# Kernel optimization log

Hardware: AMD Instinct MI355X
Metric: run time of the kernel (lower is better)

The kernel has to match this reference:

```python
import jax, jax.numpy as jnp
import numpy as np

B, N, C = 8, 1025, 1024
H = 8
D = C // H  # 128
LORA = 16
TOK = 1024

def setup_inputs() -> dict:
    key = jax.random.key(0)
    ks = jax.random.split(key, 16)
    s = 0.02
    return {
        "x": jax.random.normal(ks[0], (B, N, C), jnp.float32),
        "style_k": jax.random.normal(ks[1], (B, N, C), jnp.float32),
        "style_v": jax.random.normal(ks[2], (B, N, C), jnp.float32),
        "W_qkv": jax.random.normal(ks[3], (C, 3 * C), jnp.float32) * s,
        "W_proj": jax.random.normal(ks[4], (C, C), jnp.float32) * s,
        "b_proj": jnp.zeros((C,), jnp.float32),
        "ak": jax.random.normal(ks[5], (TOK, LORA), jnp.float32) * s,
        "bk": jax.random.normal(ks[6], (LORA, C), jnp.float32) * s,
        "av": jax.random.normal(ks[7], (TOK, LORA), jnp.float32) * s,
        "bv": jax.random.normal(ks[8], (LORA, C), jnp.float32) * s,
        "W1": jax.random.normal(ks[9], (C, C // 4), jnp.float32) * s,
        "b1": jnp.zeros((C // 4,), jnp.float32),
        "W2": jax.random.normal(ks[10], (C // 4, 1), jnp.float32) * s,
        "b2": jnp.zeros((1,), jnp.float32),
    }

def reference(x, style_k, style_v, W_qkv, W_proj, b_proj, ak, bk, av, bv, W1, b1, W2, b2):
    Bx, Nx, Cx = x.shape
    # cls-token gating MLP over transposed patch tokens: cp has shape [B, C, N-1], N-1 == C
    cls_token = x[:, :1, :]                         # [B,1,C]
    cp = jnp.transpose(x[:, 1:, :], (0, 2, 1))      # [B,C,N-1]
    h = jax.nn.relu(cp @ W1 + b1)                   # [B,C,C//4]
    attn_w = jax.nn.sigmoid(h @ W2 + b2)            # [B,C,1]
    attn_w = attn_w[..., 0][:, None, :]             # [B,1,C]
    weighted_cls = cls_token * attn_w               # [B,1,C]

    qkv = (x @ W_qkv).reshape(Bx, Nx, 3, H, D)
    q, k, v = qkv[:, :, 0], qkv[:, :, 1], qkv[:, :, 2]  # each [B,N,H,D]

    tokens_k = ak @ bk                              # [TOK, C] (TOK == C)
    tokens_v = av @ bv
    lora_k = (style_k @ tokens_k.T).reshape(Bx, Nx, H, D)
    lora_v = (style_v @ tokens_v.T).reshape(Bx, Nx, H, D)

    kk = k + lora_k
    vv = v + lora_v
    scale = D ** -0.5  # xformers default softmax scale
    scores = jnp.einsum('bqhd,bkhd->bhqk', q, kk) * scale
    attn = jax.nn.softmax(scores, axis=-1)
    out = jnp.einsum('bhqk,bkhd->bqhd', attn, vv).reshape(Bx, Nx, Cx)
    out = out @ W_proj + b_proj

    x_return = jnp.concatenate([out[:, :1, :] + weighted_cls, out[:, 1:, :]], axis=1)
    return (x_return, vv)
```

## Files before the change

### kernel.cpp

```cpp
#include <hip/hip_runtime.h>
#include <hip/hip_bf16.h>
#include <stdint.h>

#define B_ 8
#define N_ 1025
#define C_ 1024
#define H_ 8
#define D_ 128
#define TOK_ 1024
#define LORA_ 16
#define M_ 8200
#define NPAD_ 1032

using bf16x8 = __attribute__((ext_vector_type(8))) short;
using f32x4  = __attribute__((ext_vector_type(4))) float;
typedef unsigned short u16;

__device__ __forceinline__ u16 f2bf(float f) {
    union { float f; unsigned u; } v; v.f = f;
    unsigned r = v.u + 0x7fffu + ((v.u >> 16) & 1u);
    return (u16)(r >> 16);
}

__device__ __forceinline__ unsigned cvt_pk_bf16(float lo, float hi) {
    unsigned r;
    asm("v_cvt_pk_bf16_f32 %0, %1, %2" : "=v"(r) : "v"(lo), "v"(hi));
    return r;
}

__device__ __forceinline__ void gload16(const u16* g, u16* l) {
    __builtin_amdgcn_global_load_lds(
        (const __attribute__((address_space(1))) void*)g,
        (__attribute__((address_space(3))) void*)l, 16, 0, 0);
}

__device__ __forceinline__ int xcd_swz(int bid, int nwg) {
    int cpx = nwg >> 3;
    return (bid & 7) * cpx + (bid >> 3);
}

__global__ __launch_bounds__(256) void cast3_kernel(
    const float* __restrict__ x, const float* __restrict__ sk, const float* __restrict__ sv,
    u16* __restrict__ xb, u16* __restrict__ skb, u16* __restrict__ svb)
{
    const float* in = blockIdx.y == 0 ? x : (blockIdx.y == 1 ? sk : sv);
    u16* out = blockIdx.y == 0 ? xb : (blockIdx.y == 1 ? skb : svb);
    size_t i = (size_t)blockIdx.x * 256 + threadIdx.x;
    float4 a = *((const float4*)in + i * 2);
    float4 b = *((const float4*)in + i * 2 + 1);
    bf16x8 v;
    v[0] = (short)f2bf(a.x); v[1] = (short)f2bf(a.y);
    v[2] = (short)f2bf(a.z); v[3] = (short)f2bf(a.w);
    v[4] = (short)f2bf(b.x); v[5] = (short)f2bf(b.y);
    v[6] = (short)f2bf(b.z); v[7] = (short)f2bf(b.w);
    *(bf16x8*)(out + i * 8) = v;
}

__global__ __launch_bounds__(256) void padcast16_kernel(
    const float* __restrict__ ak, const float* __restrict__ av,
    u16* __restrict__ akp, u16* __restrict__ avp)
{
    const float* in = blockIdx.y ? av : ak;
    u16* out = blockIdx.y ? avp : akp;
    int i = blockIdx.x * 256 + threadIdx.x;
    int t = i >> 4, l = i & 15;
    out[(size_t)t * 32 + l] = f2bf(in[i]);
    out[(size_t)t * 32 + 16 + l] = 0;
}

__global__ __launch_bounds__(256) void castb_kernel(
    const float* __restrict__ bk, const float* __restrict__ bv,
    u16* __restrict__ bkb, u16* __restrict__ bvb)
{
    const float* in = blockIdx.y ? bv : bk;
    u16* out = blockIdx.y ? bvb : bkb;
    int i = blockIdx.x * 256 + threadIdx.x;
    out[i] = f2bf(in[i]);
}

__global__ __launch_bounds__(256) void lora16_mfma(
    const u16* __restrict__ skb, const u16* __restrict__ svb,
    const u16* __restrict__ bkb, const u16* __restrict__ bvb,
    u16* __restrict__ sk16p, u16* __restrict__ sv16p)
{
    const u16* sb = blockIdx.y ? svb : skb;
    const u16* bb = blockIdx.y ? bvb : bkb;
    u16* op = blockIdx.y ? sv16p : sk16p;
    const int lane = threadIdx.x & 63, wid = threadIdx.x >> 6;
    const int base = blockIdx.x * 64 + wid * 16;
    int ma = base + (lane & 15); if (ma > M_ - 1) ma = M_ - 1;
    const int l = lane & 15;
    const u16* arow = sb + (size_t)ma * C_ + (lane >> 4) * 8;
    const u16* brow = bb + (size_t)l * C_ + (lane >> 4) * 8;
    f32x4 acc = {0.f, 0.f, 0.f, 0.f};
#pragma unroll
    for (int k0 = 0; k0 < C_; k0 += 32) {
        bf16x8 af = *(const bf16x8*)(arow + k0);
        bf16x8 bf = *(const bf16x8*)(brow + k0);
        acc = __builtin_amdgcn_mfma_f32_16x16x32_bf16(af, bf, acc, 0, 0, 0);
    }
#pragma unroll
    for (int r = 0; r < 4; ++r) {
        int m = base + (lane >> 4) * 4 + r; if (m > M_ - 1) m = M_ - 1;
        op[(size_t)m * 32 + l] = f2bf(acc[r]);
        op[(size_t)m * 32 + 16 + l] = 0;
    }
}

__global__ __launch_bounds__(256) void wt_kernel(
    const float* __restrict__ in, u16* __restrict__ out, int K, int Nw)
{
    __shared__ float t[32][33];
    int n0 = blockIdx.x * 32, k0 = blockIdx.y * 32;
    int tx = threadIdx.x & 31, ty = threadIdx.x >> 5;
#pragma unroll
    for (int yy = 0; yy < 32; yy += 8)
        t[ty + yy][tx] = in[(size_t)(k0 + ty + yy) * Nw + n0 + tx];
    __syncthreads();
#pragma unroll
    for (int yy = 0; yy < 32; yy += 8)
        out[(size_t)(n0 + ty + yy) * K + k0 + tx] = f2bf(t[tx][ty + yy]);
}

__global__ __launch_bounds__(256) void xt_kernel(
    const float* __restrict__ x, u16* __restrict__ xT)
{
    __shared__ float tb[32][33];
    int t0 = blockIdx.x * 32, c0 = blockIdx.y * 32, b = blockIdx.z;
    int tx = threadIdx.x & 31, ty = threadIdx.x >> 5;
#pragma unroll
    for (int yy = 0; yy < 32; yy += 8)
        tb[ty + yy][tx] = x[((size_t)b * N_ + 1 + t0 + ty + yy) * C_ + c0 + tx];
    __syncthreads();
#pragma unroll
    for (int yy = 0; yy < 32; yy += 8)
        xT[((size_t)b * 1024 + c0 + ty + yy) * 1024 + t0 + tx] = f2bf(tb[tx][ty + yy]);
}

__global__ __launch_bounds__(256) void vvt_kernel(
    const float* __restrict__ vv, u16* __restrict__ vvT)
{
    __shared__ float t[32][33];
    int n0 = blockIdx.x * 32, d0 = blockIdx.y * 32, bh = blockIdx.z;
    int b = bh >> 3, h = bh & 7;
    int tx = threadIdx.x & 31, ty = threadIdx.x >> 5;
#pragma unroll
    for (int yy = 0; yy < 32; yy += 8) {
        int n = n0 + ty + yy; if (n > 1024) n = 1024;
        t[ty + yy][tx] = vv[((size_t)(b * N_) + n) * C_ + h * D_ + d0 + tx];
    }
    __syncthreads();
#pragma unroll
    for (int yy = 0; yy < 32; yy += 8) {
        int n = n0 + tx;
        if (n < NPAD_)
            vvT[((size_t)bh * D_ + d0 + ty + yy) * NPAD_ + n] = f2bf(t[tx][ty + yy]);
    }
}

__device__ __forceinline__ void stage_tile(
    const u16* __restrict__ base, int row0, int maxrow,
    u16* lds, int k0, int lane, int wid)
{
#pragma unroll
    for (int j = 0; j < 4; ++j) {
        int i = wid * 4 + j;
        int p = i * 1024 + 16 * lane;
        int row = p >> 7, cb = p & 127;
        int cbs = cb ^ ((row & 7) << 4);
        int gr = row0 + row; if (gr > maxrow) gr = maxrow;
        gload16(base + (size_t)gr * 1024 + k0 + (cbs >> 1), lds + i * 512);
    }
}

__device__ __forceinline__ void gemm_pass(
    const u16* __restrict__ A, const u16* __restrict__ Bt, int row0, int nb0,
    u16* As, u16* Bs, f32x4 acc[4][4],
    const int lane, const int wid, const int wr, const int wc)
{
    for (int k0 = 0; k0 < 1024; k0 += 64) {
        __syncthreads();
        stage_tile(A,  row0, M_ - 1,    As, k0, lane, wid);
        stage_tile(Bt, nb0,  (1 << 30), Bs, k0, lane, wid);
        __syncthreads();
#pragma unroll
        for (int ks = 0; ks < 2; ++ks) {
            bf16x8 af[4], bfr[4];
#pragma unroll
            for (int mi = 0; mi < 4; ++mi) {
                int r = wr * 64 + mi * 16 + (lane & 15);
                int byte = (r * 128 + ks * 64 + (lane >> 4) * 16) ^ ((r & 7) << 4);
                af[mi] = *(const bf16x8*)((const char*)As + byte);
            }
#pragma unroll
            for (int ni = 0; ni < 4; ++ni) {
                int r = wc * 64 + ni * 16 + (lane & 15);
                int byte = (r * 128 + ks * 64 + (lane >> 4) * 16) ^ ((r & 7) << 4);
                bfr[ni] = *(const bf16x8*)((const char*)Bs + byte);
            }
#pragma unroll
            for (int mi = 0; mi < 4; ++mi)
#pragma unroll
                for (int ni = 0; ni < 4; ++ni)
                    acc[mi][ni] = __builtin_amdgcn_mfma_f32_16x16x32_bf16(
                        af[mi], bfr[ni], acc[mi][ni], 0, 0, 0);
        }
    }
}

__global__ __launch_bounds__(256) void se_gemm(
    const u16* __restrict__ xT, const u16* __restrict__ W1T,
    const float* __restrict__ b1, const float* __restrict__ W2,
    const float* __restrict__ b2, const float* __restrict__ x,
    float* __restrict__ wcls)
{
    __shared__ u16 As[8192], Bs[8192];
    __shared__ float red[128];
    const int tid = threadIdx.x, lane = tid & 63, wid = tid >> 6;
    const int wr = wid >> 1, wc = wid & 1;
    const int row0 = blockIdx.x * 128;
    if (tid < 128) red[tid] = 0.f;
    const f32x4 FZ = {0.f, 0.f, 0.f, 0.f};

#pragma unroll
    for (int pass = 0; pass < 2; ++pass) {
        f32x4 acc[4][4];
#pragma unroll
        for (int mi = 0; mi < 4; ++mi)
#pragma unroll
            for (int ni = 0; ni < 4; ++ni) acc[mi][ni] = FZ;
        gemm_pass(xT, W1T, row0, pass * 128, As, Bs, acc, lane, wid, wr, wc);
#pragma unroll
        for (int mi = 0; mi < 4; ++mi) {
#pragma unroll
            for (int r = 0; r < 4; ++r) {
                float v = 0.f;
#pragma unroll
                for (int ni = 0; ni < 4; ++ni) {
                    int j = pass * 128 + wc * 64 + ni * 16 + (lane & 15);
                    float h = acc[mi][ni][r] + b1[j];
                    v += fmaxf(h, 0.f) * W2[j];
                }
#pragma unroll
                for (int off = 1; off < 16; off <<= 1) v += __shfl_xor(v, off);
                if ((lane & 15) == 0)
                    atomicAdd(&red[wr * 64 + mi * 16 + (lane >> 4) * 4 + r], v);
            }
        }
    }
    __syncthreads();
    if (tid < 128) {
        int row = row0 + tid;
        int b = row >> 10, c = row & 1023;
        float aw = 1.f / (1.f + expf(-(red[tid] + b2[0])));
        wcls[row] = x[(size_t)b * N_ * C_ + c] * aw;
    }
}

__global__ __launch_bounds__(256) void qkv_gemm(
    const u16* __restrict__ xb, const u16* __restrict__ WqkvT,
    const u16* __restrict__ sk16p, const u16* __restrict__ sv16p,
    const u16* __restrict__ akp, const u16* __restrict__ avp,
    u16* __restrict__ qb, u16* __restrict__ kkb, float* __restrict__ vvout)
{
    __shared__ u16 As[8192], Bs[8192];
    const int tid = threadIdx.x, lane = tid & 63, wid = tid >> 6;
    const int wr = wid >> 1, wc = wid & 1;
    const int swz = xcd_swz(blockIdx.x, 65 * 24);
    const int row0 = (swz / 24) * 128;
    const int ct = swz % 24, region = ct >> 3;
    const int creg = (ct & 7) * 128;
    const f32x4 FZ = {0.f, 0.f, 0.f, 0.f};
    f32x4 acc[4][4];
#pragma unroll
    for (int mi = 0; mi < 4; ++mi)
#pragma unroll
        for (int ni = 0; ni < 4; ++ni) acc[mi][ni] = FZ;

    gemm_pass(xb, WqkvT, row0, ct * 128, As, Bs, acc, lane, wid, wr, wc);

    if (region >= 1) {
        const u16* a16 = (region == 1) ? sk16p : sv16p;
        const u16* b16 = (region == 1) ? akp : avp;
        bf16x8 af2[4], bf2v[4];
#pragma unroll
        for (int mi = 0; mi < 4; ++mi) {
            int gr = row0 + wr * 64 + mi * 16 + (lane & 15);
            if (gr > M_ - 1) gr = M_ - 1;
            af2[mi] = *(const bf16x8*)(a16 + (size_t)gr * 32 + (lane >> 4) * 8);
        }
#pragma unroll
        for (int ni = 0; ni < 4; ++ni) {
            int gc = creg + wc * 64 + ni * 16 + (lane & 15);
            bf2v[ni] = *(const bf16x8*)(b16 + (size_t)gc * 32 + (lane >> 4) * 8);
        }
#pragma unroll
        for (int mi = 0; mi < 4; ++mi)
#pragma unroll
            for (int ni = 0; ni < 4; ++ni)
                acc[mi][ni] = __builtin_amdgcn_mfma_f32_16x16x32_bf16(
                    af2[mi], bf2v[ni], acc[mi][ni], 0, 0, 0);
    }

#pragma unroll
    for (int mi = 0; mi < 4; ++mi) {
#pragma unroll
        for (int r = 0; r < 4; ++r) {
            int gr = row0 + wr * 64 + mi * 16 + (lane >> 4) * 4 + r;
            if (gr >= M_) continue;
#pragma unroll
            for (int ni = 0; ni < 4; ++ni) {
                int gc = creg + wc * 64 + ni * 16 + (lane & 15);
                float v = acc[mi][ni][r];
                if (region == 0)      qb [(size_t)gr * C_ + gc] = f2bf(v);
                else if (region == 1) kkb[(size_t)gr * C_ + gc] = f2bf(v);
                else                  vvout[(size_t)gr * C_ + gc] = v;
            }
        }
    }
}

__global__ __launch_bounds__(256) void proj_gemm(
    const u16* __restrict__ ob, const u16* __restrict__ WprojT,
    const float* __restrict__ bias, const float* __restrict__ wcls,
    float* __restrict__ outp)
{
    __shared__ u16 As[8192], Bs[8192];
    const int tid = threadIdx.x, lane = tid & 63, wid = tid >> 6;
    const int wr = wid >> 1, wc = wid & 1;
    const int swz = xcd_swz(blockIdx.x, 65 * 8);
    const int row0 = (swz / 8) * 128;
    const int ct = swz % 8;
    const f32x4 FZ = {0.f, 0.f, 0.f, 0.f};
    f32x4 acc[4][4];
#pragma unroll
    for (int mi = 0; mi < 4; ++mi)
#pragma unroll
        for (int ni = 0; ni < 4; ++ni) acc[mi][ni] = FZ;

    gemm_pass(ob, WprojT, row0, ct * 128, As, Bs, acc, lane, wid, wr, wc);

#pragma unroll
    for (int mi = 0; mi < 4; ++mi) {
#pragma unroll
        for (int r = 0; r < 4; ++r) {
            int gr = row0 + wr * 64 + mi * 16 + (lane >> 4) * 4 + r;
            if (gr >= M_) continue;
#pragma unroll
            for (int ni = 0; ni < 4; ++ni) {
                int gc = ct * 128 + wc * 64 + ni * 16 + (lane & 15);
                float v = acc[mi][ni][r] + bias[gc];
                if (gr % N_ == 0) v += wcls[(gr / N_) * C_ + gc];
                outp[(size_t)gr * C_ + gc] = v;
            }
        }
    }
}

__device__ __forceinline__ void stageK(
    const u16* __restrict__ kbase, u16* Ksb, int kv0, int lane, int wid)
{
#pragma unroll
    for (int j = 0; j < 4; ++j) {
        int i = wid * 4 + j;
        int p = i * 1024 + 16 * lane;
        int row = p >> 8, cb = p & 255;
        int cbs = cb ^ ((row & 7) << 4);
        int n = kv0 + row; if (n > 1024) n = 1024;
        gload16(kbase + (size_t)n * C_ + (cbs >> 1), Ksb + i * 512);
    }
}
__device__ __forceinline__ void stageV(
    const u16* __restrict__ vbase, u16* Vsb, int kv0, int lane, int wid)
{
#pragma unroll
    for (int j = 0; j < 4; ++j) {
        int i = wid * 4 + j;
        int p = i * 1024 + 16 * lane;
        int row = p >> 7, cb = p & 127;
        int cbs = cb ^ ((row & 7) << 4);
        int st = kv0 + (cbs >> 1); if (st > NPAD_ - 8) st = NPAD_ - 8;
        gload16(vbase + (size_t)row * NPAD_ + st, Vsb + i * 512);
    }
}

__global__ __launch_bounds__(256) void attn_kernel(
    const u16* __restrict__ qb, const u16* __restrict__ kkb,
    const u16* __restrict__ vvT, u16* __restrict__ ob)
{
    __shared__ u16 Ks[2][8192];
    __shared__ u16 Vs[8192];
    __shared__ u16 Ps[4096];
    const int tid = threadIdx.x, lane = tid & 63, wid = tid >> 6;
    const int swz = xcd_swz(blockIdx.x, 17 * 64);
    const int qt = swz % 17, bh = swz / 17, b = bh >> 3, h = bh & 7;
    const int n0q = qt * 64;
    const float C2 = 0.1275006182f;
    const u16* kbase = kkb + (size_t)b * N_ * C_ + h * D_;
    const u16* vbase = vvT + (size_t)bh * D_ * NPAD_;

    bf16x8 qf[4];
    {
        int qrow = n0q + wid * 16 + (lane & 15); if (qrow > 1024) qrow = 1024;
        const u16* qbase = qb + (size_t)(b * N_ + qrow) * C_ + h * D_ + (lane >> 4) * 8;
#pragma unroll
        for (int ks = 0; ks < 4; ++ks) qf[ks] = *(const bf16x8*)(qbase + ks * 32);
    }

    const bf16x8 ones = {0x3F80, 0x3F80, 0x3F80, 0x3F80, 0x3F80, 0x3F80, 0x3F80, 0x3F80};
    float mrow[4];
    const f32x4 FZ = {0.f, 0.f, 0.f, 0.f};
    f32x4 of[8], lsacc = FZ;
#pragma unroll
    for (int r = 0; r < 4; ++r) mrow[r] = -3e38f;
#pragma unroll
    for (int ct = 0; ct < 8; ++ct) of[ct] = FZ;

    char* psb = (char*)Ps + wid * 2048;

    stageK(kbase, Ks[0], 0, lane, wid);

    for (int t = 0; t < 17; ++t) {
        const int cur = t & 1;
        const int kv0 = t * 64;
        asm volatile("s_waitcnt vmcnt(0)" ::: "memory");
        __builtin_amdgcn_s_barrier();
        __builtin_amdgcn_sched_barrier(0);
        stageV(vbase, Vs, kv0, lane, wid);
        if (t < 16) stageK(kbase, Ks[cur ^ 1], kv0 + 64, lane, wid);

        f32x4 s[4];
        __builtin_amdgcn_s_setprio(1);
#pragma unroll
        for (int jt = 0; jt < 4; ++jt) {
            f32x4 a = FZ;
#pragma unroll
            for (int ks = 0; ks < 4; ++ks) {
                int kvr = jt * 16 + (lane & 15);
                int byte = (kvr * 256 + ks * 64 + (lane >> 4) * 16) ^ ((kvr & 7) << 4);
                bf16x8 kf = *(const bf16x8*)((const char*)Ks[cur] + byte);
                a = __builtin_amdgcn_mfma_f32_16x16x32_bf16(qf[ks], kf, a, 0, 0, 0);
            }
            s[jt] = a;
        }
        __builtin_amdgcn_s_setprio(0);
#pragma unroll
        for (int jt = 0; jt < 4; ++jt) {
            f32x4 a = s[jt] * C2;
            int kvglob = kv0 + jt * 16 + (lane & 15);
            if (kvglob > 1024) { a[0] = -3e38f; a[1] = -3e38f; a[2] = -3e38f; a[3] = -3e38f; }
            s[jt] = a;
        }

        float tm[4];
        int need = 0;
#pragma unroll
        for (int r = 0; r < 4; ++r) {
            float t0 = fmaxf(fmaxf(s[0][r], s[1][r]), fmaxf(s[2][r], s[3][r]));
#pragma unroll
            for (int off = 1; off < 16; off <<= 1) t0 = fmaxf(t0, __shfl_xor(t0, off));
            tm[r] = t0;
            need |= (t0 > mrow[r] + 11.54f) ? 1 : 0;
        }
        if (__any(need)) {
            float al[4];
#pragma unroll
            for (int r = 0; r < 4; ++r) {
                float mn = fmaxf(mrow[r], tm[r]);
                al[r] = exp2f(mrow[r] - mn);
                mrow[r] = mn;
            }
#pragma unroll
            for (int ct = 0; ct < 8; ++ct)
#pragma unroll
                for (int r = 0; r < 4; ++r) of[ct][r] *= al[r];
#pragma unroll
            for (int r = 0; r < 4; ++r) lsacc[r] *= al[r];
        }
#pragma unroll
        for (int jt = 0; jt < 4; ++jt)
#pragma unroll
            for (int r = 0; r < 4; ++r) s[jt][r] = exp2f(s[jt][r] - mrow[r]);

#pragma unroll
        for (int jt = 0; jt < 4; ++jt) {
            unsigned pk01 = cvt_pk_bf16(s[jt][0], s[jt][1]);
            unsigned pk23 = cvt_pk_bf16(s[jt][2], s[jt][3]);
            int colb = (jt * 16 + (lane & 15)) * 2;
            int pr0 = (lane >> 4) * 4;
            *(u16*)(psb + ((pr0 * 128 + colb) ^ ((pr0 & 7) << 4)))           = (u16)pk01;
            *(u16*)(psb + (((pr0 + 1) * 128 + colb) ^ (((pr0 + 1) & 7) << 4))) = (u16)(pk01 >> 16);
            *(u16*)(psb + (((pr0 + 2) * 128 + colb) ^ (((pr0 + 2) & 7) << 4))) = (u16)pk23;
            *(u16*)(psb + (((pr0 + 3) * 128 + colb) ^ (((pr0 + 3) & 7) << 4))) = (u16)(pk23 >> 16);
        }

        bf16x8 pa[2];
#pragma unroll
        for (int ks2 = 0; ks2 < 2; ++ks2) {
            int prr = lane & 15;
            int byte = (prr * 128 + ks2 * 64 + (lane >> 4) * 16) ^ ((prr & 7) << 4);
            pa[ks2] = *(const bf16x8*)(psb + byte);
        }

        if (t < 16) asm volatile("s_waitcnt vmcnt(4)" ::: "memory");
        else        asm volatile("s_waitcnt vmcnt(0)" ::: "memory");
        __builtin_amdgcn_s_barrier();
        __builtin_amdgcn_sched_barrier(0);

        __builtin_amdgcn_s_setprio(1);
        lsacc = __builtin_amdgcn_mfma_f32_16x16x32_bf16(pa[0], ones, lsacc, 0, 0, 0);
        lsacc = __builtin_amdgcn_mfma_f32_16x16x32_bf16(pa[1], ones, lsacc, 0, 0, 0);
#pragma unroll
        for (int ct = 0; ct < 8; ++ct)
#pragma unroll
            for (int ks2 = 0; ks2 < 2; ++ks2) {
                int d = ct * 16 + (lane & 15);
                int byte = (d * 128 + ks2 * 64 + (lane >> 4) * 16) ^ ((d & 7) << 4);
                bf16x8 vf = *(const bf16x8*)((const char*)Vs + byte);
                of[ct] = __builtin_amdgcn_mfma_f32_16x16x32_bf16(pa[ks2], vf, of[ct], 0, 0, 0);
            }
        __builtin_amdgcn_s_setprio(0);
    }

#pragma unroll
    for (int ct = 0; ct < 8; ++ct)
#pragma unroll
        for (int r = 0; r < 4; ++r) {
            int n = n0q + wid * 16 + (lane >> 4) * 4 + r;
            if (n <= 1024)
                ob[(size_t)(b * N_ + n) * C_ + h * D_ + ct * 16 + (lane & 15)] =
                    f2bf(of[ct][r] / lsacc[r]);
        }
}

extern "C" void kernel_launch(void* const* d_in, const int* in_sizes, int n_in,
                              void* d_out, int out_size, void* d_ws, size_t ws_size,
                              hipStream_t stream)
{
    const float* x       = (const float*)d_in[0];
    const float* style_k = (const float*)d_in[1];
    const float* style_v = (const float*)d_in[2];
    const float* W_qkv   = (const float*)d_in[3];
    const float* W_proj  = (const float*)d_in[4];
    const float* b_proj  = (const float*)d_in[5];
    const float* ak      = (const float*)d_in[6];
    const float* bk      = (const float*)d_in[7];
    const float* av      = (const float*)d_in[8];
    const float* bv      = (const float*)d_in[9];
    const float* W1      = (const float*)d_in[10];
    const float* b1      = (const float*)d_in[11];
    const float* W2      = (const float*)d_in[12];
    const float* b2      = (const float*)d_in[13];

    float* outp   = (float*)d_out;
    float* vv_out = outp + (size_t)M_ * C_;

    u16* WqkvT = (u16*)outp;
    u16* xbb   = WqkvT + (size_t)3072 * 1024;
    u16* W1T   = xbb + (size_t)M_ * C_;
    u16* akp   = W1T + (size_t)256 * 1024;
    u16* avp   = akp + 1024 * 32;
    u16* bkb   = avp + 1024 * 32;
    u16* bvb   = bkb + 16 * 1024;
    u16* sk16p = bvb + 16 * 1024;
    u16* sv16p = sk16p + (size_t)M_ * 32;

    u16* ws     = (u16*)d_ws;
    u16* qb     = ws;
    u16* kkb    = qb  + (size_t)M_ * C_;
    u16* obuf   = kkb + (size_t)M_ * C_;
    u16* vvT    = obuf + (size_t)M_ * C_;
    u16* WprojT = vvT + (size_t)B_ * H_ * D_ * NPAD_;
    float* wcls = (float*)(WprojT + (size_t)1024 * 1024);
    u16* skb = obuf;
    u16* svb = vvT;
    u16* xT  = qb;

    wt_kernel<<<dim3(96, 32), 256, 0, stream>>>(W_qkv, WqkvT, 1024, 3072);
    wt_kernel<<<dim3(32, 32), 256, 0, stream>>>(W_proj, WprojT, 1024, 1024);
    wt_kernel<<<dim3(8, 32), 256, 0, stream>>>(W1, W1T, 1024, 256);
    padcast16_kernel<<<dim3(64, 2), 256, 0, stream>>>(ak, av, akp, avp);
    castb_kernel<<<dim3(64, 2), 256, 0, stream>>>(bk, bv, bkb, bvb);
    cast3_kernel<<<dim3(4100, 3), 256, 0, stream>>>(x, style_k, style_v, xbb, skb, svb);
    xt_kernel<<<dim3(32, 32, 8), 256, 0, stream>>>(x, xT);
    se_gemm<<<dim3(64), 256, 0, stream>>>(xT, W1T, b1, W2, b2, x, wcls);
    lora16_mfma<<<dim3(129, 2), 256, 0, stream>>>(skb, svb, bkb, bvb, sk16p, sv16p);

    qkv_gemm<<<dim3(65 * 24), 256, 0, stream>>>(xbb, WqkvT, sk16p, sv16p, akp, avp,
                                                qb, kkb, vv_out);
    vvt_kernel<<<dim3(33, 4, 64), 256, 0, stream>>>(vv_out, vvT);
    attn_kernel<<<dim3(17 * 64), 256, 0, stream>>>(qb, kkb, vvT, obuf);
    proj_gemm<<<dim3(65 * 8), 256, 0, stream>>>(obuf, WprojT, b_proj, wcls, outp);
}
```

Measured before the change: 365.7 us.

## Single-buffer K tile, raise occupancy, and cheapen the softmax rescale check

Drops the double-buffered K shared tile so K and V for the current block are loaded together between two __syncthreads, and adds a min-blocks hint of 4 to launch_bounds to raise occupancy. The online-softmax rescale check now uses one shuffle-reduced max per lane group, and per-row reductions run only when a rescale is needed. It also restricts the padding mask to the last tile and adds an extra XOR bit to the P-buffer swizzle to cut LDS bank conflicts. In exchange it gives up the overlap of the next K load with current compute and may add register pressure or spills under the tighter occupancy bound.

New measurement: 501.3 us. 1.37x slower.

```diff
diff --git a/kernel.cpp b/kernel.cpp
--- a/kernel.cpp
+++ b/kernel.cpp
@@ -384,11 +384,15 @@
     }
 }
 
-__global__ __launch_bounds__(256) void attn_kernel(
+__device__ __forceinline__ int psw(int pr, int colb) {
+    return (pr * 128 + colb) ^ ((pr & 7) << 4) ^ ((pr & 8) << 2);
+}
+
+__global__ __launch_bounds__(256, 4) void attn_kernel(
     const u16* __restrict__ qb, const u16* __restrict__ kkb,
     const u16* __restrict__ vvT, u16* __restrict__ ob)
 {
-    __shared__ u16 Ks[2][8192];
+    __shared__ u16 Ks[8192];
     __shared__ u16 Vs[8192];
     __shared__ u16 Ps[4096];
     const int tid = threadIdx.x, lane = tid & 63, wid = tid >> 6;
@@ -396,6 +400,7 @@
     const int qt = swz % 17, bh = swz / 17, b = bh >> 3, h = bh & 7;
     const int n0q = qt * 64;
     const float C2 = 0.1275006182f;
+    const float THR = 11.54f;
     const u16* kbase = kkb + (size_t)b * N_ * C_ + h * D_;
     const u16* vbase = vvT + (size_t)bh * D_ * NPAD_;
 
@@ -418,16 +423,12 @@
 
     char* psb = (char*)Ps + wid * 2048;
 
-    stageK(kbase, Ks[0], 0, lane, wid);
-
     for (int t = 0; t < 17; ++t) {
-        const int cur = t & 1;
         const int kv0 = t * 64;
-        asm volatile("s_waitcnt vmcnt(0)" ::: "memory");
-        __builtin_amdgcn_s_barrier();
-        __builtin_amdgcn_sched_barrier(0);
+        __syncthreads();
+        stageK(kbase, Ks, kv0, lane, wid);
         stageV(vbase, Vs, kv0, lane, wid);
-        if (t < 16) stageK(kbase, Ks[cur ^ 1], kv0 + 64, lane, wid);
+        __syncthreads();
 
         f32x4 s[4];
         __builtin_amdgcn_s_setprio(1);
@@ -438,35 +439,42 @@
             for (int ks = 0; ks < 4; ++ks) {
                 int kvr = jt * 16 + (lane & 15);
                 int byte = (kvr * 256 + ks * 64 + (lane >> 4) * 16) ^ ((kvr & 7) << 4);
-                bf16x8 kf = *(const bf16x8*)((const char*)Ks[cur] + byte);
+                bf16x8 kf = *(const bf16x8*)((const char*)Ks + byte);
                 a = __builtin_amdgcn_mfma_f32_16x16x32_bf16(qf[ks], kf, a, 0, 0, 0);
             }
-            s[jt] = a;
+            s[jt] = a * C2;
         }
         __builtin_amdgcn_s_setprio(0);
-#pragma unroll
-        for (int jt = 0; jt < 4; ++jt) {
-            f32x4 a = s[jt] * C2;
-            int kvglob = kv0 + jt * 16 + (lane & 15);
-            if (kvglob > 1024) { a[0] = -3e38f; a[1] = -3e38f; a[2] = -3e38f; a[3] = -3e38f; }
-            s[jt] = a;
-        }
-
-        float tm[4];
+        if (t == 16) {
+#pragma unroll
+            for (int jt = 0; jt < 4; ++jt) {
+                int kvglob = kv0 + jt * 16 + (lane & 15);
+                if (kvglob > 1024) {
+                    s[jt][0] = -3e38f; s[jt][1] = -3e38f;
+                    s[jt][2] = -3e38f; s[jt][3] = -3e38f;
+                }
+            }
+        }
+
+        float rmax[4];
+#pragma unroll
+        for (int r = 0; r < 4; ++r)
+            rmax[r] = fmaxf(fmaxf(s[0][r], s[1][r]), fmaxf(s[2][r], s[3][r]));
+        float g = fmaxf(fmaxf(rmax[0], rmax[1]), fmaxf(rmax[2], rmax[3]));
+#pragma unroll
+        for (int off = 1; off < 16; off <<= 1) g = fmaxf(g, __shfl_xor(g, off));
         int need = 0;
 #pragma unroll
-        for (int r = 0; r < 4; ++r) {
-            float t0 = fmaxf(fmaxf(s[0][r], s[1][r]), fmaxf(s[2][r], s[3][r]));
-#pragma unroll
-            for (int off = 1; off < 16; off <<= 1) t0 = fmaxf(t0, __shfl_xor(t0, off));
-            tm[r] = t0;
-            need |= (t0 > mrow[r] + 11.54f) ? 1 : 0;
-        }
+        for (int r = 0; r < 4; ++r) need |= (g > mrow[r] + THR) ? 1 : 0;
+
         if (__any(need)) {
             float al[4];
 #pragma unroll
             for (int r = 0; r < 4; ++r) {
-                float mn = fmaxf(mrow[r], tm[r]);
+                float t0 = rmax[r];
+#pragma unroll
+                for (int off = 1; off < 16; off <<= 1) t0 = fmaxf(t0, __shfl_xor(t0, off));
+                float mn = fmaxf(mrow[r], t0);
                 al[r] = exp2f(mrow[r] - mn);
                 mrow[r] = mn;
             }
@@ -488,24 +496,18 @@
             unsigned pk23 = cvt_pk_bf16(s[jt][2], s[jt][3]);
             int colb = (jt * 16 + (lane & 15)) * 2;
             int pr0 = (lane >> 4) * 4;
-            *(u16*)(psb + ((pr0 * 128 + colb) ^ ((pr0 & 7) << 4)))           = (u16)pk01;
-            *(u16*)(psb + (((pr0 + 1) * 128 + colb) ^ (((pr0 + 1) & 7) << 4))) = (u16)(pk01 >> 16);
-            *(u16*)(psb + (((pr0 + 2) * 128 + colb) ^ (((pr0 + 2) & 7) << 4))) = (u16)pk23;
-            *(u16*)(psb + (((pr0 + 3) * 128 + colb) ^ (((pr0 + 3) & 7) << 4))) = (u16)(pk23 >> 16);
+            *(u16*)(psb + psw(pr0,     colb)) = (u16)pk01;
+            *(u16*)(psb + psw(pr0 + 1, colb)) = (u16)(pk01 >> 16);
+            *(u16*)(psb + psw(pr0 + 2, colb)) = (u16)pk23;
+            *(u16*)(psb + psw(pr0 + 3, colb)) = (u16)(pk23 >> 16);
         }
 
         bf16x8 pa[2];
 #pragma unroll
         for (int ks2 = 0; ks2 < 2; ++ks2) {
             int prr = lane & 15;
-            int byte = (prr * 128 + ks2 * 64 + (lane >> 4) * 16) ^ ((prr & 7) << 4);
-            pa[ks2] = *(const bf16x8*)(psb + byte);
-        }
-
-        if (t < 16) asm volatile("s_waitcnt vmcnt(4)" ::: "memory");
-        else        asm volatile("s_waitcnt vmcnt(0)" ::: "memory");
-        __builtin_amdgcn_s_barrier();
-        __builtin_amdgcn_sched_barrier(0);
+            pa[ks2] = *(const bf16x8*)(psb + psw(prr, ks2 * 64 + (lane >> 4) * 16));
+        }
 
         __builtin_amdgcn_s_setprio(1);
         lsacc = __builtin_amdgcn_mfma_f32_16x16x32_bf16(pa[0], ones, lsacc, 0, 0, 0);
```
